# Optimization experiments

Hardware: AMD Instinct MI355X
Metric: run time of the kernel (lower is better)

## Reference

```python
import jax, jax.numpy as jnp
import numpy as np

FILTER_WIDTH = 23
NSIG = 9.0
RATIO = 4.0
SUB_LOW_RATIO = 1.0
PCT = 3.0  # normalization_percentile_threshold


def _gaussian_kernel_2d(ksize, sigma):
    # matches cv2.getGaussianKernel for sigma > 0: normalized 1D gaussian, outer product
    i = np.arange(ksize, dtype=np.float64) - (ksize - 1) / 2.0
    k1 = np.exp(-(i ** 2) / (2.0 * sigma ** 2))
    k1 /= k1.sum()
    k2 = np.outer(k1, k1)
    return k2.astype(np.float32)


def setup_inputs() -> dict:
    key = jax.random.key(0)
    k1, k2 = jax.random.split(key)
    x = jax.random.normal(k1, (16, 3, 512, 512), dtype=jnp.float32)
    mask = jax.random.uniform(k2, (16, 1, 512, 512), dtype=jnp.float32)
    kernel = jnp.asarray(_gaussian_kernel_2d(FILTER_WIDTH, NSIG))[None, None]  # [1,1,23,23]
    return {"x": x, "mask": mask, "kernel": kernel}


def reference(x, mask, kernel):
    N, C, H, W = x.shape
    pad = FILTER_WIDTH // 2  # 11

    # --- median padding (torch.median = lower median -> sorted index (n-1)//2) ---
    flat = x.reshape(N, C, H * W)
    med = jnp.sort(flat, axis=-1)[:, :, (H * W - 1) // 2] + 0.2  # [N,C]
    med = med[:, :, None, None]
    xp = mask * x + (1.0 - mask) * med  # [N,C,H,W]

    # --- Gaussian low-pass: replication pad + depthwise conv (same kernel per channel) ---
    xpad = jnp.pad(xp, ((0, 0), (0, 0), (pad, pad), (pad, pad)), mode="edge")
    k = jnp.broadcast_to(kernel, (C, 1, FILTER_WIDTH, FILTER_WIDTH))
    gauss = jax.lax.conv_general_dilated(
        xpad, k, window_strides=(1, 1), padding="VALID", feature_group_count=C
    )  # [N,C,H,W]

    res = RATIO * (xp - SUB_LOW_RATIO * gauss)

    # --- per-(n,c) percentile normalization on 1/256-quantized copy ---
    temp = jnp.trunc(res * 256.0) / 256.0  # torch .int() truncates toward zero
    tflat = temp.reshape(N, C, H * W)
    lo = jnp.percentile(tflat, PCT, axis=-1)[:, :, None, None]
    hi = jnp.percentile(tflat, 100.0 - PCT, axis=-1)[:, :, None, None]
    res = (res - lo) / (hi - lo)

    # sub_mask=True
    return res * mask
```

## Files before the change

### kernel.cpp

```cpp
#include <hip/hip_runtime.h>

#define HW 262144
#define WID 512
#define PLANES 48
#define NCH 3
#define PAD 11
#define FW 23
#define XS 92
#define HS 64

__global__ __launch_bounds__(256) void hist1_kernel(const float* __restrict__ x,
                                                    int* __restrict__ ghist1) {
  __shared__ int h[8192];
  const int p = blockIdx.x, s = blockIdx.y, tid = threadIdx.x;
  for (int i = tid; i < 8192; i += 256) h[i] = 0;
  __syncthreads();
  const float4* xv = (const float4*)(x + (size_t)p * HW + (size_t)s * (HW / 16));
#define H1(c) { int b = (int)(((c) + 8.0f) * 512.0f); b = min(max(b, 0), 8191); atomicAdd(&h[b], 1); }
  for (int i = tid; i < HW / 16 / 4; i += 256) {
    float4 v = xv[i];
    H1(v.x); H1(v.y); H1(v.z); H1(v.w);
  }
#undef H1
  __syncthreads();
  int* gh = ghist1 + p * 8192;
  const int st = (s * 512) & 8191;
  for (int k = tid; k < 8192; k += 256) {
    int i = (k + st) & 8191;
    int c = h[i];
    if (c) atomicAdd(&gh[i], c);
  }
}

__global__ __launch_bounds__(256) void scan_med_kernel(const int* __restrict__ ghist1,
                                                       float* __restrict__ med,
                                                       const float* __restrict__ kern,
                                                       float* __restrict__ k1g) {
  __shared__ int incl[256];
  __shared__ int s_chunk, s_base;
  const int p = blockIdx.x, t = threadIdx.x;
  if (p == 0 && t < FW) k1g[t] = kern[t * FW + PAD] / sqrtf(kern[PAD * FW + PAD]);
  const int* gh = ghist1 + p * 8192;
  int mysum = 0;
#pragma unroll
  for (int j = 0; j < 32; ++j) mysum += gh[t * 32 + j];
  incl[t] = mysum;
  __syncthreads();
  for (int off = 1; off < 256; off <<= 1) {
    int v = (t >= off) ? incl[t - off] : 0;
    __syncthreads();
    incl[t] += v;
    __syncthreads();
  }
  const int rank = 131072;
  {
    int excl = incl[t] - mysum;
    if (excl < rank && rank <= incl[t]) { s_chunk = t; s_base = rank - excl; }
  }
  __syncthreads();
  if (t < 64) {
    const int c = s_chunk, base = s_base;
    int cnt = (t < 32) ? gh[c * 32 + t] : 0;
    int pfx = cnt;
#pragma unroll
    for (int off = 1; off < 32; off <<= 1) {
      int u = __shfl_up(pfx, off, 64);
      if (t >= off) pfx += u;
    }
    unsigned long long m = __ballot(t < 32 && pfx >= base);
    int bin = c * 32 + (__ffsll((long long)m) - 1);
    if (t == 0) med[p] = -8.0f + ((float)bin + 0.5f) * 0.001953125f + 0.2f;
  }
}

__global__ __launch_bounds__(256) void conv_kernel(const float* __restrict__ x,
                                                   const float* __restrict__ mask,
                                                   const float* __restrict__ k1g,
                                                   const float* __restrict__ med,
                                                   float* __restrict__ res) {
  __shared__ float xs[86 * XS];
  __shared__ float hs[86 * HS];
  const int z = blockIdx.z;
  const int n = z / NCH;
  const int tbx = blockIdx.x, tby = blockIdx.y;
  const int tid = threadIdx.x;

  float k1[FW];
#pragma unroll
  for (int t = 0; t < FW; ++t) k1[t] = k1g[t];

  const float m_med = med[z];
  const int gr0 = tby * 64 - PAD;
  const int gc0 = tbx * 64 - PAD;
  const float* xb = x + (size_t)z * HW;
  const float* mb = mask + (size_t)n * HW;
  for (int i = tid; i < 86 * 86; i += 256) {
    int r = i / 86, c = i - r * 86;
    int gr = min(max(gr0 + r, 0), WID - 1);
    int gc = min(max(gc0 + c, 0), WID - 1);
    int g = gr * WID + gc;
    float xv = xb[g], mv = mb[g];
    xs[r * XS + c] = fmaf(mv, xv - m_med, m_med);
  }
  __syncthreads();

  for (int g = tid; g < 86 * 8; g += 256) {
    int r = g >> 3, c0 = (g & 7) << 3;
    const float* row = &xs[r * XS + c0];
    float w[32];
#pragma unroll
    for (int q = 0; q < 8; ++q) *(float4*)&w[q * 4] = *(const float4*)(row + q * 4);
    float a[8];
#pragma unroll
    for (int j = 0; j < 8; ++j) a[j] = 0.f;
#pragma unroll
    for (int t = 0; t < FW; ++t) {
      float k = k1[t];
#pragma unroll
      for (int j = 0; j < 8; ++j) a[j] = fmaf(k, w[t + j], a[j]);
    }
    *(float4*)&hs[r * HS + c0] = make_float4(a[0], a[1], a[2], a[3]);
    *(float4*)&hs[r * HS + c0 + 4] = make_float4(a[4], a[5], a[6], a[7]);
  }
  __syncthreads();

  const int ct = (tid & 15) << 2;
  const int rt = (tid >> 4) << 2;
  float4 acc[4];
#pragma unroll
  for (int j = 0; j < 4; ++j) acc[j] = make_float4(0.f, 0.f, 0.f, 0.f);
#pragma unroll
  for (int tp = 0; tp < 26; ++tp) {
    float4 v = *(const float4*)&hs[(rt + tp) * HS + ct];
    const int jlo = (tp - 22 > 0) ? (tp - 22) : 0;
    const int jhi = (tp < 3) ? tp : 3;
#pragma unroll
    for (int j = jlo; j <= jhi; ++j) {
      float k = k1[tp - j];
      acc[j].x = fmaf(k, v.x, acc[j].x);
      acc[j].y = fmaf(k, v.y, acc[j].y);
      acc[j].z = fmaf(k, v.z, acc[j].z);
      acc[j].w = fmaf(k, v.w, acc[j].w);
    }
  }

  float* rb = res + (size_t)z * HW + (size_t)(tby * 64) * WID + tbx * 64;
#pragma unroll
  for (int j = 0; j < 4; ++j) {
    const float* xr = &xs[(rt + j + PAD) * XS + ct];
    float4 A = *(const float4*)(xr + 8);
    float4 B = *(const float4*)(xr + 12);
    float4 o;
    o.x = 4.0f * (A.w - acc[j].x);
    o.y = 4.0f * (B.x - acc[j].y);
    o.z = 4.0f * (B.y - acc[j].z);
    o.w = 4.0f * (B.z - acc[j].w);
    *(float4*)&rb[(size_t)(rt + j) * WID + ct] = o;
  }
}

__global__ __launch_bounds__(256) void hist_kernel(const float* __restrict__ res,
                                                   int* __restrict__ ghist) {
  __shared__ int h[8192];
  const int p = blockIdx.x, s = blockIdx.y, tid = threadIdx.x;
  for (int i = tid; i < 8192; i += 256) h[i] = 0;
  __syncthreads();
  const float4* rv = (const float4*)(res + (size_t)p * HW + (size_t)s * (HW / 16));
#define HADD(c) { int b = (int)((c) * 256.0f) + 4096; b = min(max(b, 0), 8191); atomicAdd(&h[b], 1); }
  for (int i = tid; i < HW / 16 / 4; i += 256) {
    float4 v = rv[i];
    HADD(v.x); HADD(v.y); HADD(v.z); HADD(v.w);
  }
#undef HADD
  __syncthreads();
  int* gh = ghist + p * 8192;
  const int st = (s * 512) & 8191;
  for (int k = tid; k < 8192; k += 256) {
    int i = (k + st) & 8191;
    int c = h[i];
    if (c) atomicAdd(&gh[i], c);
  }
}

__global__ __launch_bounds__(256) void pct_kernel(const int* __restrict__ ghist,
                                                  float* __restrict__ lo_out,
                                                  float* __restrict__ inv_out) {
  __shared__ int incl[256];
  __shared__ int s_chunk, s_base;
  __shared__ float s_v[4];
  const int p = blockIdx.x, t = threadIdx.x;
  const int* gh = ghist + p * 8192;
  int mysum = 0;
#pragma unroll
  for (int j = 0; j < 32; ++j) mysum += gh[t * 32 + j];
  incl[t] = mysum;
  __syncthreads();
  for (int off = 1; off < 256; off <<= 1) {
    int v = (t >= off) ? incl[t - off] : 0;
    __syncthreads();
    incl[t] += v;
    __syncthreads();
  }
  const int ranks[4] = {7865, 7866, 254279, 254280};
#pragma unroll
  for (int r = 0; r < 4; ++r) {
    const int rank = ranks[r];
    int excl = incl[t] - mysum;
    if (excl < rank && rank <= incl[t]) { s_chunk = t; s_base = rank - excl; }
    __syncthreads();
    if (t < 64) {
      const int c = s_chunk, base = s_base;
      int cnt = (t < 32) ? gh[c * 32 + t] : 0;
      int pfx = cnt;
#pragma unroll
      for (int off = 1; off < 32; off <<= 1) {
        int u = __shfl_up(pfx, off, 64);
        if (t >= off) pfx += u;
      }
      unsigned long long m = __ballot(t < 32 && pfx >= base);
      int bin = c * 32 + (__ffsll((long long)m) - 1);
      if (t == 0) s_v[r] = (float)(bin - 4096) * 0.00390625f;
    }
    __syncthreads();
  }
  if (t == 0) {
    const double fl = 0.29, fh = 0.71;
    double lov = (double)s_v[0] + fl * ((double)s_v[1] - (double)s_v[0]);
    double hiv = (double)s_v[2] + fh * ((double)s_v[3] - (double)s_v[2]);
    lo_out[p] = (float)lov;
    inv_out[p] = (float)(1.0 / (hiv - lov));
  }
}

__global__ __launch_bounds__(256) void final_kernel(float* __restrict__ res,
                                                    const float* __restrict__ mask,
                                                    const float* __restrict__ lo,
                                                    const float* __restrict__ inv) {
  const int i = blockIdx.x * 256 + threadIdx.x;
  const int e = i << 2;
  const int z = e >> 18;
  const int n = z / NCH;
  const int hw = e & (HW - 1);
  float4 r = ((const float4*)res)[i];
  float4 m = *(const float4*)(mask + (size_t)n * HW + hw);
  const float l = lo[z];
  const float iv = inv[z];
  float4 o;
  o.x = (r.x - l) * iv * m.x;
  o.y = (r.y - l) * iv * m.y;
  o.z = (r.z - l) * iv * m.z;
  o.w = (r.w - l) * iv * m.w;
  ((float4*)res)[i] = o;
}

extern "C" void kernel_launch(void* const* d_in, const int* in_sizes, int n_in,
                              void* d_out, int out_size, void* d_ws, size_t ws_size,
                              hipStream_t stream) {
  (void)in_sizes; (void)n_in; (void)out_size; (void)ws_size;
  const float* x = (const float*)d_in[0];
  const float* mask = (const float*)d_in[1];
  const float* kern = (const float*)d_in[2];
  float* out = (float*)d_out;

  int* hist = (int*)d_ws;
  int* ghist1 = hist + PLANES * 8192;
  float* med = (float*)(ghist1 + PLANES * 8192);
  float* lo = med + PLANES;
  float* inv = lo + PLANES;
  float* k1g = inv + PLANES;

  hipMemsetAsync(hist, 0, (size_t)PLANES * (8192 + 8192) * sizeof(int), stream);
  hist1_kernel<<<dim3(PLANES, 16), 256, 0, stream>>>(x, ghist1);
  scan_med_kernel<<<PLANES, 256, 0, stream>>>(ghist1, med, kern, k1g);
  conv_kernel<<<dim3(8, 8, PLANES), 256, 0, stream>>>(x, mask, k1g, med, out);
  hist_kernel<<<dim3(PLANES, 16), 256, 0, stream>>>(out, hist);
  pct_kernel<<<PLANES, 256, 0, stream>>>(hist, lo, inv);
  final_kernel<<<(HW * PLANES / 4 + 255) / 256, 256, 0, stream>>>(out, mask, lo, inv);
}
```

Before: 213.2 us.

## Fuse percentile histogram into conv kernel and reuse shared memory buffer

Folds the histogram pass into the convolution kernel: each 64x64 tile bins its outputs into a shared 8192-bin histogram and flushes it to the global per-plane histogram with atomics. This removes one kernel launch and a full re-read of the result tensor. The horizontal pass results are now held in registers so they can be written back into the same shared buffer, and the xp centre values are recomputed from global x and mask instead of read from shared memory. In exchange there are 3072 blocks each flushing up to 8192 global atomics (versus 768 before), plus extra syncs and shared-memory zeroing per tile.

```diff
diff --git a/kernel.cpp b/kernel.cpp
--- a/kernel.cpp
+++ b/kernel.cpp
@@ -7,7 +7,10 @@
 #define PAD 11
 #define FW 23
 #define XS 92
-#define HS 64
+
+__device__ __forceinline__ float uniform_f(float v) {
+  return __uint_as_float((unsigned)__builtin_amdgcn_readfirstlane((int)__float_as_uint(v)));
+}
 
 __global__ __launch_bounds__(256) void hist1_kernel(const float* __restrict__ x,
                                                     int* __restrict__ ghist1) {
@@ -77,9 +80,10 @@
                                                    const float* __restrict__ mask,
                                                    const float* __restrict__ k1g,
                                                    const float* __restrict__ med,
-                                                   float* __restrict__ res) {
-  __shared__ float xs[86 * XS];
-  __shared__ float hs[86 * HS];
+                                                   float* __restrict__ res,
+                                                   int* __restrict__ ghist) {
+  __shared__ int sbuf[8192];
+  float* xsf = (float*)sbuf;
   const int z = blockIdx.z;
   const int n = z / NCH;
   const int tbx = blockIdx.x, tby = blockIdx.y;
@@ -87,9 +91,9 @@
 
   float k1[FW];
 #pragma unroll
-  for (int t = 0; t < FW; ++t) k1[t] = k1g[t];
-
-  const float m_med = med[z];
+  for (int t = 0; t < FW; ++t) k1[t] = uniform_f(k1g[t]);
+
+  const float m_med = uniform_f(med[z]);
   const int gr0 = tby * 64 - PAD;
   const int gc0 = tbx * 64 - PAD;
   const float* xb = x + (size_t)z * HW;
@@ -100,27 +104,40 @@
     int gc = min(max(gc0 + c, 0), WID - 1);
     int g = gr * WID + gc;
     float xv = xb[g], mv = mb[g];
-    xs[r * XS + c] = fmaf(mv, xv - m_med, m_med);
-  }
-  __syncthreads();
-
-  for (int g = tid; g < 86 * 8; g += 256) {
-    int r = g >> 3, c0 = (g & 7) << 3;
-    const float* row = &xs[r * XS + c0];
-    float w[32];
-#pragma unroll
-    for (int q = 0; q < 8; ++q) *(float4*)&w[q * 4] = *(const float4*)(row + q * 4);
-    float a[8];
-#pragma unroll
-    for (int j = 0; j < 8; ++j) a[j] = 0.f;
-#pragma unroll
-    for (int t = 0; t < FW; ++t) {
-      float k = k1[t];
-#pragma unroll
-      for (int j = 0; j < 8; ++j) a[j] = fmaf(k, w[t + j], a[j]);
-    }
-    *(float4*)&hs[r * HS + c0] = make_float4(a[0], a[1], a[2], a[3]);
-    *(float4*)&hs[r * HS + c0 + 4] = make_float4(a[4], a[5], a[6], a[7]);
+    xsf[r * XS + c] = fmaf(mv, xv - m_med, m_med);
+  }
+  __syncthreads();
+
+  float ah[3][8];
+#pragma unroll
+  for (int it = 0; it < 3; ++it) {
+    const int g = tid + (it << 8);
+    if (g < 86 * 8) {
+      const int r = g >> 3, c0 = (g & 7) << 3;
+      const float* row = &xsf[r * XS + c0];
+      float w[32];
+#pragma unroll
+      for (int q = 0; q < 8; ++q) *(float4*)&w[q * 4] = *(const float4*)(row + q * 4);
+#pragma unroll
+      for (int j = 0; j < 8; ++j) ah[it][j] = 0.f;
+#pragma unroll
+      for (int t = 0; t < FW; ++t) {
+        const float k = k1[t];
+#pragma unroll
+        for (int j = 0; j < 8; ++j) ah[it][j] = fmaf(k, w[t + j], ah[it][j]);
+      }
+    }
+  }
+  __syncthreads();
+
+#pragma unroll
+  for (int it = 0; it < 3; ++it) {
+    const int g = tid + (it << 8);
+    if (g < 86 * 8) {
+      const int r = g >> 3, c0 = (g & 7) << 3;
+      *(float4*)&xsf[r * XS + c0] = make_float4(ah[it][0], ah[it][1], ah[it][2], ah[it][3]);
+      *(float4*)&xsf[r * XS + c0 + 4] = make_float4(ah[it][4], ah[it][5], ah[it][6], ah[it][7]);
+    }
   }
   __syncthreads();
 
@@ -131,7 +148,7 @@
   for (int j = 0; j < 4; ++j) acc[j] = make_float4(0.f, 0.f, 0.f, 0.f);
 #pragma unroll
   for (int tp = 0; tp < 26; ++tp) {
-    float4 v = *(const float4*)&hs[(rt + tp) * HS + ct];
+    float4 v = *(const float4*)&xsf[(rt + tp) * XS + ct];
     const int jlo = (tp - 22 > 0) ? (tp - 22) : 0;
     const int jhi = (tp < 3) ? tp : 3;
 #pragma unroll
@@ -144,41 +161,43 @@
     }
   }
 
-  float* rb = res + (size_t)z * HW + (size_t)(tby * 64) * WID + tbx * 64;
+  const int orow = tby * 64 + rt;
+  const int ocol = tbx * 64 + ct;
+  float4 xv[4], mv[4];
 #pragma unroll
   for (int j = 0; j < 4; ++j) {
-    const float* xr = &xs[(rt + j + PAD) * XS + ct];
-    float4 A = *(const float4*)(xr + 8);
-    float4 B = *(const float4*)(xr + 12);
+    const size_t g = (size_t)(orow + j) * WID + ocol;
+    xv[j] = *(const float4*)(xb + g);
+    mv[j] = *(const float4*)(mb + g);
+  }
+  __syncthreads();
+  for (int i = tid; i < 8192; i += 256) sbuf[i] = 0;
+  __syncthreads();
+
+  float* rb = res + (size_t)z * HW + (size_t)orow * WID + ocol;
+#define HADD(c) { int b = (int)((c) * 256.0f) + 4096; b = min(max(b, 0), 8191); atomicAdd(&sbuf[b], 1); }
+#pragma unroll
+  for (int j = 0; j < 4; ++j) {
     float4 o;
-    o.x = 4.0f * (A.w - acc[j].x);
-    o.y = 4.0f * (B.x - acc[j].y);
-    o.z = 4.0f * (B.y - acc[j].z);
-    o.w = 4.0f * (B.z - acc[j].w);
-    *(float4*)&rb[(size_t)(rt + j) * WID + ct] = o;
-  }
-}
-
-__global__ __launch_bounds__(256) void hist_kernel(const float* __restrict__ res,
-                                                   int* __restrict__ ghist) {
-  __shared__ int h[8192];
-  const int p = blockIdx.x, s = blockIdx.y, tid = threadIdx.x;
-  for (int i = tid; i < 8192; i += 256) h[i] = 0;
-  __syncthreads();
-  const float4* rv = (const float4*)(res + (size_t)p * HW + (size_t)s * (HW / 16));
-#define HADD(c) { int b = (int)((c) * 256.0f) + 4096; b = min(max(b, 0), 8191); atomicAdd(&h[b], 1); }
-  for (int i = tid; i < HW / 16 / 4; i += 256) {
-    float4 v = rv[i];
-    HADD(v.x); HADD(v.y); HADD(v.z); HADD(v.w);
+    o.x = 4.0f * (fmaf(mv[j].x, xv[j].x - m_med, m_med) - acc[j].x);
+    o.y = 4.0f * (fmaf(mv[j].y, xv[j].y - m_med, m_med) - acc[j].y);
+    o.z = 4.0f * (fmaf(mv[j].z, xv[j].z - m_med, m_med) - acc[j].z);
+    o.w = 4.0f * (fmaf(mv[j].w, xv[j].w - m_med, m_med) - acc[j].w);
+    HADD(o.x); HADD(o.y); HADD(o.z); HADD(o.w);
+    *(float4*)(rb + (size_t)j * WID) = o;
   }
 #undef HADD
   __syncthreads();
-  int* gh = ghist + p * 8192;
-  const int st = (s * 512) & 8191;
-  for (int k = tid; k < 8192; k += 256) {
-    int i = (k + st) & 8191;
-    int c = h[i];
-    if (c) atomicAdd(&gh[i], c);
+
+  int* gh = ghist + z * 8192;
+  const int st = ((tby * 8 + tbx) << 7) & 8191;
+  for (int k4 = tid; k4 < 2048; k4 += 256) {
+    const int i = ((k4 << 2) + st) & 8191;
+    const int4 c4 = *(const int4*)&sbuf[i];
+    if (c4.x) atomicAdd(&gh[i], c4.x);
+    if (c4.y) atomicAdd(&gh[i + 1], c4.y);
+    if (c4.z) atomicAdd(&gh[i + 2], c4.z);
+    if (c4.w) atomicAdd(&gh[i + 3], c4.w);
   }
 }
 
@@ -272,8 +291,7 @@
   hipMemsetAsync(hist, 0, (size_t)PLANES * (8192 + 8192) * sizeof(int), stream);
   hist1_kernel<<<dim3(PLANES, 16), 256, 0, stream>>>(x, ghist1);
   scan_med_kernel<<<PLANES, 256, 0, stream>>>(ghist1, med, kern, k1g);
-  conv_kernel<<<dim3(8, 8, PLANES), 256, 0, stream>>>(x, mask, k1g, med, out);
-  hist_kernel<<<dim3(PLANES, 16), 256, 0, stream>>>(out, hist);
+  conv_kernel<<<dim3(8, 8, PLANES), 256, 0, stream>>>(x, mask, k1g, med, out, hist);
   pct_kernel<<<PLANES, 256, 0, stream>>>(hist, lo, inv);
   final_kernel<<<(HW * PLANES / 4 + 255) / 256, 256, 0, stream>>>(out, mask, lo, inv);
 }
```

New measurement: 333.4 us. 56.4% more time.
